# Kernel optimization log

Measured on AMD Instinct MI355X. Metric: run time of the kernel, lower is better.

## Reference

```python
import jax, jax.numpy as jnp
import numpy as np

T, B = 256, 256
OBS, FEAT, A = 512, 512, 15
H = FEAT + A + 1  # lstm_output_size = feature_dim + num_actions + 1 = 528


def setup_inputs() -> dict:
    key = jax.random.key(0)
    ks = jax.random.split(key, 16)
    s = 0.05
    f32 = jnp.float32
    return {
        "obs": jax.random.normal(ks[0], (T, B, OBS), f32),
        "last_action": jax.random.randint(ks[1], (T, B), 0, A, dtype=jnp.int32),
        "reward": jax.random.normal(ks[2], (T, B), f32),
        "terminated": jax.random.bernoulli(ks[3], 0.05, (T, B)),
        # encoder Linear(OBS -> FEAT)
        "W_enc": jax.random.normal(ks[4], (FEAT, OBS), f32) * s,
        "b_enc": jnp.zeros((FEAT,), f32),
        # 2-layer LSTM, input size == hidden size == H, torch gate order i,f,g,o
        "w_ih0": jax.random.normal(ks[5], (4 * H, H), f32) * s,
        "w_hh0": jax.random.normal(ks[6], (4 * H, H), f32) * s,
        "b_ih0": jnp.zeros((4 * H,), f32),
        "b_hh0": jnp.zeros((4 * H,), f32),
        "w_ih1": jax.random.normal(ks[7], (4 * H, H), f32) * s,
        "w_hh1": jax.random.normal(ks[8], (4 * H, H), f32) * s,
        "b_ih1": jnp.zeros((4 * H,), f32),
        "b_hh1": jnp.zeros((4 * H,), f32),
        # heads
        "W_pol": jax.random.normal(ks[9], (A, H), f32) * s,
        "b_pol": jnp.zeros((A,), f32),
        "W_base": jax.random.normal(ks[10], (1, H), f32) * s,
        "b_base": jnp.zeros((1,), f32),
    }


def reference(obs, last_action, reward, terminated,
              W_enc, b_enc,
              w_ih0, w_hh0, b_ih0, b_hh0,
              w_ih1, w_hh1, b_ih1, b_hh1,
              W_pol, b_pol, W_base, b_base):
    Tn, Bn = obs.shape[0], obs.shape[1]
    feats = jax.nn.relu(jnp.einsum('tbo,fo->tbf', obs, W_enc) + b_enc)
    one_hot = jax.nn.one_hot(last_action, A, dtype=feats.dtype)
    clipped_r = jnp.clip(reward, -1.0, 1.0)[..., None]
    x = jnp.concatenate([feats, clipped_r, one_hot], axis=-1)  # [T,B,H]
    nd = (~terminated).astype(x.dtype)[..., None]              # [T,B,1]

    w_ih = (w_ih0, w_ih1)
    w_hh = (w_hh0, w_hh1)
    b_ih = (b_ih0, b_ih1)
    b_hh = (b_hh0, b_hh1)

    def step(carry, inp):
        h, c = carry          # each [2,B,H]
        x_t, nd_t = inp       # [B,H], [B,1]
        h = h * nd_t          # done-mask reset of state, per original loop
        c = c * nd_t
        inp_l = x_t
        new_h, new_c = [], []
        for l in range(2):
            gates = inp_l @ w_ih[l].T + b_ih[l] + h[l] @ w_hh[l].T + b_hh[l]
            i, f, g, o = jnp.split(gates, 4, axis=-1)
            c_l = jax.nn.sigmoid(f) * c[l] + jax.nn.sigmoid(i) * jnp.tanh(g)
            h_l = jax.nn.sigmoid(o) * jnp.tanh(c_l)
            new_h.append(h_l)
            new_c.append(c_l)
            inp_l = h_l
        return (jnp.stack(new_h), jnp.stack(new_c)), inp_l

    h0 = jnp.zeros((2, Bn, H), x.dtype)  # init_state: zeros
    c0 = jnp.zeros((2, Bn, H), x.dtype)
    (hT, cT), lstm_out = jax.lax.scan(step, (h0, c0), (x, nd))  # lstm_out [T,B,H]

    policy_logits = lstm_out @ W_pol.T + b_pol          # [T,B,A]
    baseline = (lstm_out @ W_base.T + b_base)[..., 0]   # [T,B]
    action = jax.random.categorical(jax.random.key(1), policy_logits, axis=-1)  # [T,B]
    return policy_logits, baseline, action, hT, cT
```

## Files before the change

kernel.cpp:

```cpp
#include <hip/hip_runtime.h>
#include <stdint.h>
#include <math.h>

#define TSTEPS 256
#define BATCH  256
#define OBS_D  512
#define FEATD  512
#define NACT   15
#define HDIM   528
#define HB     (HDIM*BATCH)

#define OFF_ND    0
#define OFF_FLAG  65536
#define ALW_BYTES 262208
#define SB        91952
#define FXT       (SB)
#define FH0       (FXT + 4*HB)
#define FH1       (FH0 + 2*HB)
#define FC0       (FH1 + 2*HB)
#define FC1       (FC0 + HB)

#define DBS0   0
#define DBS1   2112
#define DBENC  4224
#define DHW    4736
#define DHB    13184
#define DALW_N 13200

#define OUT_POL   0
#define OUT_BASE  983040
#define OUT_ACT   1048576
#define OUT_H     1114112
#define OUT_C     1384448

__device__ __forceinline__ float sigf_(float x){ return 1.0f/(1.0f+expf(-x)); }

__device__ __forceinline__ uint32_t rotl32_(uint32_t x, uint32_t d){
  return (x<<d)|(x>>(32u-d));
}

__device__ double gumbel_for(uint32_t idx){
  uint32_t x0 = 0u, x1 = idx;
  const uint32_t k0 = 0u, k1 = 1u;
  const uint32_t ks[3] = {k0, k1, 0x1BD11BDAu ^ k0 ^ k1};
  x0 += ks[0]; x1 += ks[1];
  const uint32_t R0[4] = {13u,15u,26u,6u}, R1[4] = {17u,29u,16u,24u};
  #pragma unroll
  for (int g=0; g<5; ++g){
    const uint32_t* r = (g&1) ? R1 : R0;
    #pragma unroll
    for (int j=0;j<4;++j){ x0 += x1; x1 = rotl32_(x1, r[j]); x1 ^= x0; }
    x0 += ks[(g+1)%3];
    x1 += ks[(g+2)%3] + (uint32_t)(g+1);
  }
  const uint32_t bits = x0 ^ x1;
  float u = __uint_as_float((bits>>9) | 0x3f800000u) - 1.0f;
  const float TINY = 1.17549435e-38f;
  u = u * (1.0f - TINY) + TINY;
  u = fmaxf(TINY, u);
  return -log(-log((double)u));
}

__global__ void zero_kernel(float* __restrict__ p, int n){
  int i = blockIdx.x*256 + threadIdx.x;
  if (i < n) p[i] = 0.0f;
}

__global__ void detect_term_kernel(const void* __restrict__ term, int* __restrict__ flag){
  __shared__ int s_nf, s_nb, s_ni;
  if (threadIdx.x==0){ s_nf=0; s_nb=0; s_ni=0; }
  __syncthreads();
  const uint8_t*  pb = (const uint8_t*)term;
  const uint32_t* pw = (const uint32_t*)term;
  int nf=0, nb=0, ni=0;
  for (int i=threadIdx.x; i<16384; i+=256){
    uint32_t v = pw[i];
    if (v == 0x3F800000u) nf++;
    if (v == 1u) ni++;
  }
  for (int o=threadIdx.x; o<65536; o+=256){
    if ((o&3) && pb[o]) nb++;
  }
  if (nf) atomicAdd(&s_nf, nf);
  if (nb) atomicAdd(&s_nb, nb);
  if (ni) atomicAdd(&s_ni, ni);
  __syncthreads();
  if (threadIdx.x==0){
    flag[0] = (s_nf>0) ? 2 : ((s_nb>0) ? 0 : ((s_ni>0) ? 1 : 0));
  }
}

__global__ void nd_kernel(const void* __restrict__ term, const int* __restrict__ flag,
                          float* __restrict__ nd){
  int i = blockIdx.x*256 + threadIdx.x;
  if (i >= TSTEPS*BATCH) return;
  int f = flag[0];
  bool done;
  if (f == 0)      done = ((const uint8_t*)term)[i] != 0;
  else if (f == 1) done = ((const int*)term)[i] != 0;
  else             done = ((const float*)term)[i] != 0.0f;
  nd[i] = done ? 0.0f : 1.0f;
}

__global__ void prep_small_kernel(float* __restrict__ alw,
    const float* __restrict__ bih0, const float* __restrict__ bhh0,
    const float* __restrict__ bih1, const float* __restrict__ bhh1,
    const float* __restrict__ benc,
    const float* __restrict__ Wpol, const float* __restrict__ bpol,
    const float* __restrict__ Wbase, const float* __restrict__ bbase){
  int i = blockIdx.x*256 + threadIdx.x;
  if (i >= DALW_N) return;
  if (i < 2112)            alw[DBS0 + i] = bih0[i] + bhh0[i];
  else if (i < 4224)       { int j=i-2112; alw[DBS1 + j] = bih1[j] + bhh1[j]; }
  else if (i < 4736)       { int j=i-4224; alw[DBENC + j] = benc[j]; }
  else if (i < 13184)      { int j=i-4736; int r=j/HDIM, k=j%HDIM;
                             alw[DHW + j] = (r<NACT ? Wpol[r*HDIM+k] : Wbase[k]); }
  else                     { int j=i-13184; alw[DHB + j] = (j<NACT ? bpol[j] : bbase[0]); }
}

__device__ __forceinline__ void lstm_block(
    float* __restrict__ smem,
    int jt, int step, const float* __restrict__ srcA, const float* __restrict__ srcB,
    const float* __restrict__ wih, const float* __restrict__ whh,
    const float* __restrict__ bsum,
    const float* __restrict__ nd, float* __restrict__ cbuf, float* __restrict__ hout,
    int b)
{
  const int j0 = jt*2;

  {
    for (int i = b; i < 2112; i += 256){
      const int c  = i / 264;
      const int r4 = i - c*264;
      const int col = (c>>1)*HDIM + j0 + (c&1);
      float4 v;
      if (r4 < 132) v = *(const float4*)(wih + (size_t)col*HDIM + r4*4);
      else          v = *(const float4*)(whh + (size_t)col*HDIM + (r4-132)*4);
      *(float4*)(smem + c*1056 + r4*4) = v;
    }
  }
  __syncthreads();

  const float ndv = nd[step*BATCH + b];
  float acc[8];
  #pragma unroll
  for (int c=0;c<8;++c) acc[c] = bsum[(c>>1)*HDIM + j0 + (c&1)];

  {
    const float* a = srcA + b;
    #pragma unroll 2
    for (int kq=0; kq<132; ++kq){
      float xv[4];
      #pragma unroll
      for (int u=0;u<4;++u) xv[u] = a[(size_t)(kq*4+u)*BATCH];
      #pragma unroll
      for (int c=0;c<8;++c){
        const float4 w4 = *(const float4*)(smem + c*1056 + kq*4);
        acc[c] = fmaf(w4.x, xv[0], acc[c]);
        acc[c] = fmaf(w4.y, xv[1], acc[c]);
        acc[c] = fmaf(w4.z, xv[2], acc[c]);
        acc[c] = fmaf(w4.w, xv[3], acc[c]);
      }
    }
  }

  {
    const float* bb = srcB + b;
    #pragma unroll 2
    for (int kq=0; kq<132; ++kq){
      float hv[4];
      #pragma unroll
      for (int u=0;u<4;++u) hv[u] = bb[(size_t)(kq*4+u)*BATCH] * ndv;
      #pragma unroll
      for (int c=0;c<8;++c){
        const float4 w4 = *(const float4*)(smem + c*1056 + 528 + kq*4);
        acc[c] = fmaf(w4.x, hv[0], acc[c]);
        acc[c] = fmaf(w4.y, hv[1], acc[c]);
        acc[c] = fmaf(w4.z, hv[2], acc[c]);
        acc[c] = fmaf(w4.w, hv[3], acc[c]);
      }
    }
  }

  #pragma unroll
  for (int jj=0;jj<2;++jj){
    const float gi=acc[0+jj], gf=acc[2+jj], gg=acc[4+jj], go=acc[6+jj];
    const int idx=(j0+jj)*BATCH+b;
    const float cold = cbuf[idx]*ndv;
    const float cn = sigf_(gf)*cold + sigf_(gi)*tanhf(gg);
    const float hn = sigf_(go)*tanhf(cn);
    cbuf[idx]=cn; hout[idx]=hn;
  }
}

__global__ __launch_bounds__(256) void step_kernel(
  const float* __restrict__ obs, const int* __restrict__ lastAct,
  const float* __restrict__ reward,
  const float* __restrict__ wenc,
  const float* __restrict__ wih0, const float* __restrict__ whh0,
  const float* __restrict__ wih1, const float* __restrict__ whh1,
  float* __restrict__ ws, float* __restrict__ alw,
  float* __restrict__ out, int t)
{
  __shared__ float smem[8448];
  const int bid = blockIdx.x;
  const int b = threadIdx.x;
  float* nd = ws + OFF_ND;
  float* xT = ws + FXT;
  float* h0 = ws + FH0;
  float* h1 = ws + FH1;
  float* c0 = ws + FC0;
  float* c1 = ws + FC1;

  if (bid < 264) {
    if (t < 0 || t > 255) return;
    lstm_block(smem, bid, t,
               xT + (size_t)(t&3)*HB,
               h0 + (size_t)((t+1)&1)*HB,
               wih0, whh0, alw + DBS0, nd, c0,
               h0 + (size_t)(t&1)*HB, b);
  } else if (bid < 528) {
    const int s = t - 1;
    if (s < 0 || s > 255) return;
    lstm_block(smem, bid-264, s,
               h0 + (size_t)(s&1)*HB,
               h1 + (size_t)((s+1)&1)*HB,
               wih1, whh1, alw + DBS1, nd, c1,
               h1 + (size_t)(s&1)*HB, b);
  } else if (bid < 593) {
    const int te = t + 2;
    if (te < 0 || te > 255) return;
    float* xs = xT + (size_t)(te&3)*HB;
    if (bid < 592) {
      float (*lx)[257] = (float(*)[257])smem;
      const int e = bid - 528;
      const int f0 = e*8;
      float acc[8];
      const float* wrow[8];
      #pragma unroll
      for (int c=0;c<8;++c){ acc[c]=alw[DBENC+f0+c]; wrow[c]=wenc+(size_t)(f0+c)*OBS_D; }
      const int r0 = threadIdx.x>>3;
      const int kk = (threadIdx.x&7)<<2;
      for (int kc=0; kc<OBS_D; kc+=32){
        __syncthreads();
        #pragma unroll
        for (int rr=0; rr<256; rr+=32){
          const float4 v = *(const float4*)(obs + ((size_t)te*BATCH + (r0+rr))*OBS_D + kc + kk);
          lx[kk+0][r0+rr]=v.x; lx[kk+1][r0+rr]=v.y; lx[kk+2][r0+rr]=v.z; lx[kk+3][r0+rr]=v.w;
        }
        __syncthreads();
        #pragma unroll 4
        for (int k2=0;k2<32;++k2){
          const float xv = lx[k2][b];
          #pragma unroll
          for (int c=0;c<8;++c) acc[c] = fmaf(xv, wrow[c][kc+k2], acc[c]);
        }
      }
      #pragma unroll
      for (int c=0;c<8;++c) xs[(size_t)(f0+c)*BATCH + b] = fmaxf(acc[c], 0.0f);
    } else {
      const float r = reward[te*BATCH + b];
      xs[(size_t)FEATD*BATCH + b] = fminf(fmaxf(r, -1.0f), 1.0f);
      const int la = lastAct[te*BATCH + b];
      #pragma unroll
      for (int a2=0; a2<NACT; ++a2)
        xs[(size_t)(FEATD+1+a2)*BATCH + b] = (a2==la) ? 1.0f : 0.0f;
    }
  } else {
    const int s = t - 2;
    if (s < 0 || s > 255) return;
    const float* hsrc = h1 + (size_t)(s&1)*HB;
    float acc[16];
    #pragma unroll
    for (int c=0;c<16;++c) acc[c]=alw[DHB+c];
    const float* hb = hsrc + b;
    #pragma unroll 4
    for (int k=0;k<HDIM;++k){
      const float hv = hb[(size_t)k*BATCH];
      #pragma unroll
      for (int c=0;c<16;++c) acc[c] = fmaf(hv, alw[DHW + (size_t)c*HDIM + k], acc[c]);
    }
    const int row = s*BATCH + b;
    #pragma unroll
    for (int c=0;c<15;++c) out[OUT_POL + (size_t)row*NACT + c] = acc[c];
    out[OUT_BASE + row] = acc[15];
    double best = -1.0e300; int bi = 0;
    #pragma unroll
    for (int a2=0; a2<NACT; ++a2){
      const double v = (double)acc[a2] + gumbel_for((uint32_t)(row*NACT + a2));
      if (v > best){ best = v; bi = a2; }
    }
    out[OUT_ACT + row] = (float)bi;
  }
}

__global__ void finalize_kernel(const float* __restrict__ ws, float* __restrict__ out){
  int i = blockIdx.x*256 + threadIdx.x;
  if (i >= 2*HB) return;
  const int l = i / HB;
  const int r = i % HB;
  const int bq = r / HDIM;
  const int j  = r % HDIM;
  const float* hf = ws + (l==0 ? FH0 : FH1) + HB;
  const float* cf = ws + (l==0 ? FC0 : FC1);
  out[OUT_H + i] = hf[(size_t)j*BATCH + bq];
  out[OUT_C + i] = cf[(size_t)j*BATCH + bq];
}

extern "C" void kernel_launch(void* const* d_in, const int* in_sizes, int n_in,
                              void* d_out, int out_size, void* d_ws, size_t ws_size,
                              hipStream_t stream) {
  const float* obs     = (const float*)d_in[0];
  const int*   lastAct = (const int*)  d_in[1];
  const float* reward  = (const float*)d_in[2];
  const void*  term    =               d_in[3];
  const float* Wenc    = (const float*)d_in[4];
  const float* benc    = (const float*)d_in[5];
  const float* wih0    = (const float*)d_in[6];
  const float* whh0    = (const float*)d_in[7];
  const float* bih0    = (const float*)d_in[8];
  const float* bhh0    = (const float*)d_in[9];
  const float* wih1    = (const float*)d_in[10];
  const float* whh1    = (const float*)d_in[11];
  const float* bih1    = (const float*)d_in[12];
  const float* bhh1    = (const float*)d_in[13];
  const float* Wpol    = (const float*)d_in[14];
  const float* bpol    = (const float*)d_in[15];
  const float* Wbase   = (const float*)d_in[16];
  const float* bbase   = (const float*)d_in[17];
  float*  ws   = (float*)d_ws;
  int*    flag = (int*)(ws + OFF_FLAG);
  float*  alw  = (float*)((char*)d_ws + ALW_BYTES);
  float*  out  = (float*)d_out;

  {
    const int nz = 6*HB;
    zero_kernel<<<(nz+255)/256, 256, 0, stream>>>(ws + FH0, nz);
  }
  detect_term_kernel<<<1, 256, 0, stream>>>(term, flag);
  nd_kernel<<<(TSTEPS*BATCH+255)/256, 256, 0, stream>>>(term, flag, ws + OFF_ND);
  prep_small_kernel<<<(DALW_N+255)/256, 256, 0, stream>>>(alw,
      bih0, bhh0, bih1, bhh1, benc, Wpol, bpol, Wbase, bbase);

  for (int t = -2; t <= 257; ++t) {
    step_kernel<<<594, 256, 0, stream>>>(
      obs, lastAct, reward,
      Wenc, wih0, whh0, wih1, whh1,
      ws, alw, out, t);
  }
  finalize_kernel<<<(2*HB+255)/256, 256, 0, stream>>>(ws, out);
}
```

Baseline: 20.73 ms.

## Split LSTM gate GEMV across two thread halves with shared-memory reduction

Each LSTM block now launches 512 threads: one half computes the input-weight contribution and the other the recurrent-weight contribution, then partial sums are combined through shared memory before the gate nonlinearity. The aim is to halve the serial dot-product length per thread and raise the number of wavefronts in flight on the latency-bound per-step kernel. The encoder and head blocks now leave half their threads idle, and the change adds an extra barrier and shared-memory traffic, with higher register pressure under 512-thread launch bounds.

```diff
diff --git a/kernel.cpp b/kernel.cpp
--- a/kernel.cpp
+++ b/kernel.cpp
@@ -118,82 +118,90 @@
   else                     { int j=i-13184; alw[DHB + j] = (j<NACT ? bpol[j] : bbase[0]); }
 }
 
-__device__ __forceinline__ void lstm_block(
-    float* __restrict__ smem,
+__device__ __forceinline__ void lstm_split(
+    float* __restrict__ smw,
+    float* __restrict__ smr,
     int jt, int step, const float* __restrict__ srcA, const float* __restrict__ srcB,
     const float* __restrict__ wih, const float* __restrict__ whh,
     const float* __restrict__ bsum,
     const float* __restrict__ nd, float* __restrict__ cbuf, float* __restrict__ hout,
-    int b)
+    int tid)
 {
+  const int pass = tid >> 8;
+  const int b = tid & 255;
   const int j0 = jt*2;
 
-  {
-    for (int i = b; i < 2112; i += 256){
-      const int c  = i / 264;
-      const int r4 = i - c*264;
-      const int col = (c>>1)*HDIM + j0 + (c&1);
-      float4 v;
-      if (r4 < 132) v = *(const float4*)(wih + (size_t)col*HDIM + r4*4);
-      else          v = *(const float4*)(whh + (size_t)col*HDIM + (r4-132)*4);
-      *(float4*)(smem + c*1056 + r4*4) = v;
-    }
+  for (int i = tid; i < 2112; i += 512){
+    const int c  = i / 264;
+    const int r4 = i - c*264;
+    const int col = (c>>1)*HDIM + j0 + (c&1);
+    float4 v;
+    if (r4 < 132) v = *(const float4*)(wih + (size_t)col*HDIM + r4*4);
+    else          v = *(const float4*)(whh + (size_t)col*HDIM + (r4-132)*4);
+    *(float4*)(smw + c*1056 + r4*4) = v;
   }
   __syncthreads();
 
   const float ndv = nd[step*BATCH + b];
   float acc[8];
-  #pragma unroll
-  for (int c=0;c<8;++c) acc[c] = bsum[(c>>1)*HDIM + j0 + (c&1)];
-
-  {
+
+  if (pass == 0){
+    #pragma unroll
+    for (int c=0;c<8;++c) acc[c] = bsum[(c>>1)*HDIM + j0 + (c&1)];
     const float* a = srcA + b;
-    #pragma unroll 2
+    #pragma unroll 4
     for (int kq=0; kq<132; ++kq){
       float xv[4];
       #pragma unroll
       for (int u=0;u<4;++u) xv[u] = a[(size_t)(kq*4+u)*BATCH];
       #pragma unroll
       for (int c=0;c<8;++c){
-        const float4 w4 = *(const float4*)(smem + c*1056 + kq*4);
+        const float4 w4 = *(const float4*)(smw + c*1056 + kq*4);
         acc[c] = fmaf(w4.x, xv[0], acc[c]);
         acc[c] = fmaf(w4.y, xv[1], acc[c]);
         acc[c] = fmaf(w4.z, xv[2], acc[c]);
         acc[c] = fmaf(w4.w, xv[3], acc[c]);
       }
     }
-  }
-
-  {
+  } else {
+    #pragma unroll
+    for (int c=0;c<8;++c) acc[c] = 0.0f;
     const float* bb = srcB + b;
-    #pragma unroll 2
+    #pragma unroll 4
     for (int kq=0; kq<132; ++kq){
       float hv[4];
       #pragma unroll
       for (int u=0;u<4;++u) hv[u] = bb[(size_t)(kq*4+u)*BATCH] * ndv;
       #pragma unroll
       for (int c=0;c<8;++c){
-        const float4 w4 = *(const float4*)(smem + c*1056 + 528 + kq*4);
+        const float4 w4 = *(const float4*)(smw + c*1056 + 528 + kq*4);
         acc[c] = fmaf(w4.x, hv[0], acc[c]);
         acc[c] = fmaf(w4.y, hv[1], acc[c]);
         acc[c] = fmaf(w4.z, hv[2], acc[c]);
         acc[c] = fmaf(w4.w, hv[3], acc[c]);
       }
     }
-  }
-
-  #pragma unroll
-  for (int jj=0;jj<2;++jj){
-    const float gi=acc[0+jj], gf=acc[2+jj], gg=acc[4+jj], go=acc[6+jj];
-    const int idx=(j0+jj)*BATCH+b;
-    const float cold = cbuf[idx]*ndv;
-    const float cn = sigf_(gf)*cold + sigf_(gi)*tanhf(gg);
-    const float hn = sigf_(go)*tanhf(cn);
-    cbuf[idx]=cn; hout[idx]=hn;
-  }
-}
-
-__global__ __launch_bounds__(256) void step_kernel(
+    #pragma unroll
+    for (int c=0;c<8;++c) smr[c*257 + b] = acc[c];
+  }
+  __syncthreads();
+
+  if (pass == 0){
+    #pragma unroll
+    for (int c=0;c<8;++c) acc[c] += smr[c*257 + b];
+    #pragma unroll
+    for (int jj=0;jj<2;++jj){
+      const float gi=acc[0+jj], gf=acc[2+jj], gg=acc[4+jj], go=acc[6+jj];
+      const int idx=(j0+jj)*BATCH+b;
+      const float cold = cbuf[idx]*ndv;
+      const float cn = sigf_(gf)*cold + sigf_(gi)*tanhf(gg);
+      const float hn = sigf_(go)*tanhf(cn);
+      cbuf[idx]=cn; hout[idx]=hn;
+    }
+  }
+}
+
+__global__ __launch_bounds__(512) void step_kernel(
   const float* __restrict__ obs, const int* __restrict__ lastAct,
   const float* __restrict__ reward,
   const float* __restrict__ wenc,
@@ -202,9 +210,10 @@
   float* __restrict__ ws, float* __restrict__ alw,
   float* __restrict__ out, int t)
 {
-  __shared__ float smem[8448];
+  __shared__ float smw[8448];
+  __shared__ float smr[8*257];
   const int bid = blockIdx.x;
-  const int b = threadIdx.x;
+  const int tid = threadIdx.x;
   float* nd = ws + OFF_ND;
   float* xT = ws + FXT;
   float* h0 = ws + FH0;
@@ -214,61 +223,69 @@
 
   if (bid < 264) {
     if (t < 0 || t > 255) return;
-    lstm_block(smem, bid, t,
+    lstm_split(smw, smr, bid, t,
                xT + (size_t)(t&3)*HB,
                h0 + (size_t)((t+1)&1)*HB,
                wih0, whh0, alw + DBS0, nd, c0,
-               h0 + (size_t)(t&1)*HB, b);
+               h0 + (size_t)(t&1)*HB, tid);
   } else if (bid < 528) {
     const int s = t - 1;
     if (s < 0 || s > 255) return;
-    lstm_block(smem, bid-264, s,
+    lstm_split(smw, smr, bid-264, s,
                h0 + (size_t)(s&1)*HB,
                h1 + (size_t)((s+1)&1)*HB,
                wih1, whh1, alw + DBS1, nd, c1,
-               h1 + (size_t)(s&1)*HB, b);
+               h1 + (size_t)(s&1)*HB, tid);
   } else if (bid < 593) {
     const int te = t + 2;
     if (te < 0 || te > 255) return;
     float* xs = xT + (size_t)(te&3)*HB;
     if (bid < 592) {
-      float (*lx)[257] = (float(*)[257])smem;
+      float (*lx)[257] = (float(*)[257])smw;
       const int e = bid - 528;
       const int f0 = e*8;
       float acc[8];
       const float* wrow[8];
       #pragma unroll
       for (int c=0;c<8;++c){ acc[c]=alw[DBENC+f0+c]; wrow[c]=wenc+(size_t)(f0+c)*OBS_D; }
-      const int r0 = threadIdx.x>>3;
-      const int kk = (threadIdx.x&7)<<2;
+      const int r0 = tid>>3;
+      const int kk = (tid&7)<<2;
+      const int b = tid & 255;
       for (int kc=0; kc<OBS_D; kc+=32){
         __syncthreads();
         #pragma unroll
-        for (int rr=0; rr<256; rr+=32){
+        for (int rr=0; rr<256; rr+=64){
           const float4 v = *(const float4*)(obs + ((size_t)te*BATCH + (r0+rr))*OBS_D + kc + kk);
           lx[kk+0][r0+rr]=v.x; lx[kk+1][r0+rr]=v.y; lx[kk+2][r0+rr]=v.z; lx[kk+3][r0+rr]=v.w;
         }
         __syncthreads();
-        #pragma unroll 4
-        for (int k2=0;k2<32;++k2){
-          const float xv = lx[k2][b];
-          #pragma unroll
-          for (int c=0;c<8;++c) acc[c] = fmaf(xv, wrow[c][kc+k2], acc[c]);
+        if (tid < 256){
+          #pragma unroll 4
+          for (int k2=0;k2<32;++k2){
+            const float xv = lx[k2][b];
+            #pragma unroll
+            for (int c=0;c<8;++c) acc[c] = fmaf(xv, wrow[c][kc+k2], acc[c]);
+          }
         }
       }
-      #pragma unroll
-      for (int c=0;c<8;++c) xs[(size_t)(f0+c)*BATCH + b] = fmaxf(acc[c], 0.0f);
+      if (tid < 256){
+        #pragma unroll
+        for (int c=0;c<8;++c) xs[(size_t)(f0+c)*BATCH + tid] = fmaxf(acc[c], 0.0f);
+      }
     } else {
-      const float r = reward[te*BATCH + b];
-      xs[(size_t)FEATD*BATCH + b] = fminf(fmaxf(r, -1.0f), 1.0f);
-      const int la = lastAct[te*BATCH + b];
-      #pragma unroll
-      for (int a2=0; a2<NACT; ++a2)
-        xs[(size_t)(FEATD+1+a2)*BATCH + b] = (a2==la) ? 1.0f : 0.0f;
+      if (tid < 256){
+        const float r = reward[te*BATCH + tid];
+        xs[(size_t)FEATD*BATCH + tid] = fminf(fmaxf(r, -1.0f), 1.0f);
+        const int la = lastAct[te*BATCH + tid];
+        #pragma unroll
+        for (int a2=0; a2<NACT; ++a2)
+          xs[(size_t)(FEATD+1+a2)*BATCH + tid] = (a2==la) ? 1.0f : 0.0f;
+      }
     }
   } else {
     const int s = t - 2;
-    if (s < 0 || s > 255) return;
+    if (s < 0 || s > 255 || tid >= 256) return;
+    const int b = tid;
     const float* hsrc = h1 + (size_t)(s&1)*HB;
     float acc[16];
     #pragma unroll
@@ -343,7 +360,7 @@
       bih0, bhh0, bih1, bhh1, benc, Wpol, bpol, Wbase, bbase);
 
   for (int t = -2; t <= 257; ++t) {
-    step_kernel<<<594, 256, 0, stream>>>(
+    step_kernel<<<594, 512, 0, stream>>>(
       obs, lastAct, reward,
       Wenc, wih0, whh0, wih1, whh1,
       ws, alw, out, t);
```

Measured after the change: 34.70 ms. 1.67x slower.
